# Kernel tuning notes

Measured on AMD Instinct MI355X. Metric: run time of the kernel, lower is better.

The kernel has to match this reference:

```python
import jax, jax.numpy as jnp
import numpy as np

S, L = 4096, 16            # words per sentence, max chars per word
DW, DC, DH = 256, 128, 512  # word emb, char emb, hidden dims
V, A, T = 50000, 128, 64    # vocab, alphabet, tagset sizes


def _lstm_cell(x, h, c, Wih, Whh, bih, bhh):
    # PyTorch LSTM gate math, gate order i, f, g, o
    gates = x @ Wih.T + h @ Whh.T + bih + bhh
    i, f, g, o = jnp.split(gates, 4, axis=-1)
    i, f, o = jax.nn.sigmoid(i), jax.nn.sigmoid(f), jax.nn.sigmoid(o)
    c = f * c + i * jnp.tanh(g)
    h = o * jnp.tanh(c)
    return h, c


def setup_inputs() -> dict:
    key = jax.random.key(0)
    ks = jax.random.split(key, 16)
    s = 0.1
    word_idxs = jax.random.randint(ks[0], (S,), 0, V)
    char_idxs = jax.random.randint(ks[1], (S, L), 0, A)
    char_lens = jnp.maximum(jax.random.randint(ks[2], (S,), 0, L + 1), 1)
    return {
        "word_idxs": word_idxs,
        "char_idxs": char_idxs,
        "char_lens": char_lens,
        "word_emb": jax.random.normal(ks[3], (V, DW)) * s,
        "char_emb": jax.random.normal(ks[4], (A, DC)) * s,
        "Wih_c": jax.random.normal(ks[5], (4 * DC, DC)) * s,
        "Whh_c": jax.random.normal(ks[6], (4 * DC, DC)) * s,
        "bih_c": jnp.zeros((4 * DC,)),
        "bhh_c": jnp.zeros((4 * DC,)),
        "Wih_w": jax.random.normal(ks[7], (4 * DH, DW + DC)) * s,
        "Whh_w": jax.random.normal(ks[8], (4 * DH, DH)) * s,
        "bih_w": jnp.zeros((4 * DH,)),
        "bhh_w": jnp.zeros((4 * DH,)),
        "W_tag": jax.random.normal(ks[9], (T, DH)) * s,
        "b_tag": jnp.zeros((T,)),
    }


def reference(word_idxs, char_idxs, char_lens,
              word_emb, char_emb,
              Wih_c, Whh_c, bih_c, bhh_c,
              Wih_w, Whh_w, bih_w, bhh_w,
              W_tag, b_tag):
    # ---- char-level LSTM, batched over all S words (replaces per-word loop) ----
    cx = char_emb[char_idxs]                 # [S, L, DC]
    cx_t = jnp.swapaxes(cx, 0, 1)            # [L, S, DC], time-major

    def char_step(carry, x_t):
        h, c = carry
        h, c = _lstm_cell(x_t, h, c, Wih_c, Whh_c, bih_c, bhh_c)
        return (h, c), h

    h0 = jnp.zeros((S, DC), cx.dtype)
    _, hs = jax.lax.scan(char_step, (h0, h0), cx_t)   # hs: [L, S, DC]
    hs = jnp.swapaxes(hs, 0, 1)                       # [S, L, DC]
    # original takes lstm_car_out[-1] at the word's true length
    char_feat = jnp.take_along_axis(
        hs, (char_lens - 1)[:, None, None], axis=1)[:, 0, :]   # [S, DC]

    # ---- word-level LSTM over the sentence (batch = 1 in original) ----
    we = word_emb[word_idxs]                          # [S, DW]
    wx = jnp.concatenate([we, char_feat], axis=-1)    # [S, DW+DC]

    def word_step(carry, x_t):
        h, c = carry
        h, c = _lstm_cell(x_t, h, c, Wih_w, Whh_w, bih_w, bhh_w)
        return (h, c), h

    wh0 = jnp.zeros((DH,), wx.dtype)
    _, wout = jax.lax.scan(word_step, (wh0, wh0), wx)  # [S, DH]

    tag_space = wout @ W_tag.T + b_tag                 # [S, T]
    # NOTE: original uses F.log_softmax(tag_space, dim=0) -- over the sequence axis
    return jax.nn.log_softmax(tag_space, axis=0)
```

## Files before the change

### kernel.cpp

```cpp
#include <hip/hip_runtime.h>
#include <hip/hip_bf16.h>


typedef short short8 __attribute__((ext_vector_type(8)));
typedef float f32x4 __attribute__((ext_vector_type(4)));

#define NUM_S 4096
#define NUM_L 16

__device__ __forceinline__ unsigned short f2bf(float f) {
  unsigned x = __float_as_uint(f);
  x += 0x7FFFu + ((x >> 16) & 1u);
  return (unsigned short)(x >> 16);
}
__device__ __forceinline__ uint4 packf8(float4 a, float4 b) {
  uint4 r;
  r.x = (unsigned)f2bf(a.x) | ((unsigned)f2bf(a.y) << 16);
  r.y = (unsigned)f2bf(a.z) | ((unsigned)f2bf(a.w) << 16);
  r.z = (unsigned)f2bf(b.x) | ((unsigned)f2bf(b.y) << 16);
  r.w = (unsigned)f2bf(b.z) | ((unsigned)f2bf(b.w) << 16);
  return r;
}
__device__ __forceinline__ short8 pack_bf8(const float* src) {
  const float4 a = *reinterpret_cast<const float4*>(src);
  const float4 b = *reinterpret_cast<const float4*>(src + 4);
  uint4 u = packf8(a, b);
  union { uint4 u; short8 s; } cv; cv.u = u;
  return cv.s;
}
__device__ __forceinline__ float sigm(float x) { return 1.0f / (1.0f + __expf(-x)); }
__device__ __forceinline__ float tanh_f(float x) {
  x = fminf(15.0f, fmaxf(-15.0f, x));
  float e = __expf(2.0f * x);
  return (e - 1.0f) / (e + 1.0f);
}

__global__ __launch_bounds__(256, 1) void char_lstm_kernel(
    const int* __restrict__ char_idxs,
    const int* __restrict__ char_lens,
    const float* __restrict__ char_emb,
    const float* __restrict__ Wih_c,
    const float* __restrict__ Whh_c,
    const float* __restrict__ bih_c,
    const float* __restrict__ bhh_c,
    float* __restrict__ char_feat)
{
  constexpr int XSTR = 264;
  __shared__ __align__(16) unsigned short X[16 * XSTR];

  const int wg = blockIdx.x;
  const int tid = threadIdx.x;
  const int lane = tid & 63;
  const int wv = tid >> 6;
  const int col = lane & 15;
  const int krow = lane >> 4;

  short8 wfrag[8][8];
#pragma unroll
  for (int p = 0; p < 8; ++p) {
    const int nt = (p >> 1) * 8 + 2 * wv + (p & 1);
    const int n = nt * 16 + col;
#pragma unroll
    for (int kt = 0; kt < 8; ++kt) {
      const int k = kt * 32 + krow * 8;
      const float* src = (kt < 4) ? (Wih_c + n * 128 + k)
                                  : (Whh_c + n * 128 + (k - 128));
      wfrag[p][kt] = pack_bf8(src);
    }
  }
  float bsum[8];
#pragma unroll
  for (int p = 0; p < 8; ++p) {
    const int nt = (p >> 1) * 8 + 2 * wv + (p & 1);
    const int n = nt * 16 + col;
    bsum[p] = bih_c[n] + bhh_c[n];
  }
  int clen[4];
#pragma unroll
  for (int r = 0; r < 4; ++r) clen[r] = char_lens[wg * 16 + krow * 4 + r];

  {
    const int m = tid >> 4, c = tid & 15;
    uint4 z; z.x = z.y = z.z = z.w = 0u;
    *reinterpret_cast<uint4*>(&X[m * XSTR + 128 + c * 8]) = z;
  }
  float cstate[8];
#pragma unroll
  for (int i = 0; i < 8; ++i) cstate[i] = 0.0f;

  for (int l = 0; l < NUM_L; ++l) {
    {
      const int m = tid >> 4, c = tid & 15;
      const int ci = char_idxs[(wg * 16 + m) * NUM_L + l];
      const float4 a = *reinterpret_cast<const float4*>(char_emb + ci * 128 + c * 8);
      const float4 b = *reinterpret_cast<const float4*>(char_emb + ci * 128 + c * 8 + 4);
      *reinterpret_cast<uint4*>(&X[m * XSTR + c * 8]) = packf8(a, b);
    }
    __syncthreads();

    short8 afr[8];
#pragma unroll
    for (int kt = 0; kt < 8; ++kt)
      afr[kt] = *reinterpret_cast<const short8*>(&X[col * XSTR + kt * 32 + krow * 8]);

    f32x4 acc[8];
#pragma unroll
    for (int p = 0; p < 8; ++p) { f32x4 v = {bsum[p], bsum[p], bsum[p], bsum[p]}; acc[p] = v; }
#pragma unroll
    for (int kt = 0; kt < 8; ++kt)
#pragma unroll
      for (int p = 0; p < 8; ++p)
        acc[p] = __builtin_amdgcn_mfma_f32_16x16x32_bf16(afr[kt], wfrag[p][kt], acc[p], 0, 0, 0);
    __syncthreads();

#pragma unroll
    for (int sub = 0; sub < 2; ++sub) {
#pragma unroll
      for (int r = 0; r < 4; ++r) {
        const int m = krow * 4 + r;
        const int d = (2 * wv + sub) * 16 + col;
        const float iv = acc[0 + sub][r];
        const float fv = acc[2 + sub][r];
        const float gv = acc[4 + sub][r];
        const float ov = acc[6 + sub][r];
        const float cc = sigm(fv) * cstate[sub * 4 + r] + sigm(iv) * tanh_f(gv);
        const float hh = sigm(ov) * tanh_f(cc);
        cstate[sub * 4 + r] = cc;
        X[m * XSTR + 128 + d] = (unsigned short)f2bf(hh);
        if (clen[r] == l + 1) char_feat[(wg * 16 + m) * 128 + d] = hh;
      }
    }
  }
}

__global__ __launch_bounds__(256) void cvt_bf16_kernel(
    const float* __restrict__ in, unsigned short* __restrict__ out, int n8) {
  const int i = blockIdx.x * 256 + threadIdx.x;
  if (i < n8) {
    const float4 a = reinterpret_cast<const float4*>(in)[2 * i];
    const float4 b = reinterpret_cast<const float4*>(in)[2 * i + 1];
    reinterpret_cast<uint4*>(out)[i] = packf8(a, b);
  }
}

__global__ __launch_bounds__(256, 1) void word_input_kernel(
    const int* __restrict__ word_idxs,
    const float* __restrict__ word_emb,
    const float* __restrict__ char_feat,
    const unsigned short* __restrict__ wih_bf,
    const float* __restrict__ bih_w,
    const float* __restrict__ bhh_w,
    float* __restrict__ xpart)
{
  constexpr int XSTR = 392;
  __shared__ __align__(16) unsigned short X[64 * XSTR];
  const int wg = blockIdx.x, tid = threadIdx.x;
  const int lane = tid & 63, wv = tid >> 6, col = lane & 15, krow = lane >> 4;
  const int t0 = wg * 64;

#pragma unroll
  for (int rr = 0; rr < 4; ++rr) {
    const int m = rr * 16 + (tid >> 4), c = tid & 15;
    const int widx = word_idxs[t0 + m];
    const float* we = word_emb + (size_t)widx * 256;
    const float4 a0 = *reinterpret_cast<const float4*>(we + c * 8);
    const float4 b0 = *reinterpret_cast<const float4*>(we + c * 8 + 4);
    *reinterpret_cast<uint4*>(&X[m * XSTR + c * 8]) = packf8(a0, b0);
    const float4 a1 = *reinterpret_cast<const float4*>(we + 128 + c * 8);
    const float4 b1 = *reinterpret_cast<const float4*>(we + 128 + c * 8 + 4);
    *reinterpret_cast<uint4*>(&X[m * XSTR + 128 + c * 8]) = packf8(a1, b1);
    const float* cf = char_feat + (size_t)(t0 + m) * 128;
    const float4 a2 = *reinterpret_cast<const float4*>(cf + c * 8);
    const float4 b2 = *reinterpret_cast<const float4*>(cf + c * 8 + 4);
    *reinterpret_cast<uint4*>(&X[m * XSTR + 256 + c * 8]) = packf8(a2, b2);
  }
  __syncthreads();

  short8 afr[4][12];
#pragma unroll
  for (int mt = 0; mt < 4; ++mt)
#pragma unroll
    for (int kt = 0; kt < 12; ++kt)
      afr[mt][kt] = *reinterpret_cast<const short8*>(
          &X[(mt * 16 + col) * XSTR + kt * 32 + krow * 8]);

  for (int nn = 0; nn < 32; ++nn) {
    const int nt = wv * 32 + nn;
    const int n = nt * 16 + col;
    const float bs = bih_w[n] + bhh_w[n];
    f32x4 acc[4];
#pragma unroll
    for (int mt = 0; mt < 4; ++mt) { f32x4 v = {bs, bs, bs, bs}; acc[mt] = v; }
#pragma unroll
    for (int kt = 0; kt < 12; ++kt) {
      const short8 bfr = *reinterpret_cast<const short8*>(
          wih_bf + (size_t)n * 384 + kt * 32 + krow * 8);
#pragma unroll
      for (int mt = 0; mt < 4; ++mt)
        acc[mt] = __builtin_amdgcn_mfma_f32_16x16x32_bf16(afr[mt][kt], bfr, acc[mt], 0, 0, 0);
    }
#pragma unroll
    for (int mt = 0; mt < 4; ++mt)
#pragma unroll
      for (int r = 0; r < 4; ++r)
        xpart[(size_t)(t0 + mt * 16 + krow * 4 + r) * 2048 + n] = acc[mt][r];
  }
}

__global__ __launch_bounds__(512, 1) void word_lstm_kernel(
    const float* __restrict__ Whh_w,
    const float* __restrict__ xpart,
    unsigned* __restrict__ hx)
{
  const int tid = threadIdx.x;
  const int wg = blockIdx.x;
  const int dim = tid >> 4;
  const int gate = (tid >> 2) & 3;
  const int seg = tid & 3;
  const int R = gate * 512 + wg * 32 + dim;

  float4 w4[32];
  {
    const float4* wrow = reinterpret_cast<const float4*>(
        Whh_w + (size_t)R * 512 + seg * 128);
#pragma unroll
    for (int i = 0; i < 32; ++i) w4[i] = wrow[(i + seg) & 31];
  }

  __shared__ __align__(16) float h_lds[2][512];
  __shared__ float glds[128];
  h_lds[0][tid] = 0.0f;
  float creg = 0.0f;
  float xp = (seg == 0) ? xpart[R] : 0.0f;
  __syncthreads();

  for (int t = 0; t < NUM_S; ++t) {
    const int cur = t & 1;

    const float4* h4 = reinterpret_cast<const float4*>(&h_lds[cur][0]) + seg * 32;
    float a0 = 0.0f, a1 = 0.0f;
#pragma unroll
    for (int jj = 0; jj < 32; jj += 2) {
      const int j0 = (jj + seg) & 31;
      const int j1 = (jj + 1 + seg) & 31;
      const float4 hA = h4[j0]; const float4 wA = w4[jj];
      const float4 hB = h4[j1]; const float4 wB = w4[jj + 1];
      a0 = fmaf(wA.x, hA.x, a0); a0 = fmaf(wA.y, hA.y, a0);
      a0 = fmaf(wA.z, hA.z, a0); a0 = fmaf(wA.w, hA.w, a0);
      a1 = fmaf(wB.x, hB.x, a1); a1 = fmaf(wB.y, hB.y, a1);
      a1 = fmaf(wB.z, hB.z, a1); a1 = fmaf(wB.w, hB.w, a1);
    }
    float acc = a0 + a1;
    acc += __shfl_xor(acc, 1, 64);
    acc += __shfl_xor(acc, 2, 64);
    if (seg == 0) {
      glds[gate * 32 + dim] = acc + xp;
      if (t + 1 < NUM_S) xp = xpart[(size_t)(t + 1) * 2048 + R];
    }
    __syncthreads();

    if (tid < 64) {
      unsigned hb = 0u;
      if (tid < 32) {
        const float iv = glds[tid];
        const float fv = glds[32 + tid];
        const float gv = glds[64 + tid];
        const float ov = glds[96 + tid];
        const float cc = sigm(fv) * creg + sigm(iv) * tanh_f(gv);
        const float hh = sigm(ov) * tanh_f(cc);
        creg = cc;
        hb = __float_as_uint(hh) + 0x40000000u;
      }
      const unsigned lo = __shfl(hb, (tid & 15) * 2, 64);
      const unsigned hi = __shfl(hb, (tid & 15) * 2 + 1, 64);
      if (tid < 16) {
        const unsigned long long pv =
            (unsigned long long)lo | ((unsigned long long)hi << 32);
        __hip_atomic_store(
            reinterpret_cast<unsigned long long*>(hx + (size_t)t * 512 + wg * 32) + tid,
            pv, __ATOMIC_RELAXED, __HIP_MEMORY_SCOPE_AGENT);
      }
    }

    if (t + 1 < NUM_S && tid >= 192 && tid < 448) {
      const int c = tid - 192;
      const unsigned long long* p =
          reinterpret_cast<const unsigned long long*>(hx + (size_t)t * 512) + c;
      unsigned long long v =
          __hip_atomic_load(p, __ATOMIC_RELAXED, __HIP_MEMORY_SCOPE_AGENT);
      int guard = 0;
      while (((unsigned)v == 0u || (unsigned)(v >> 32) == 0u) &&
             ++guard < (1 << 20)) {
        v = __hip_atomic_load(p, __ATOMIC_RELAXED, __HIP_MEMORY_SCOPE_AGENT);
      }
      h_lds[cur ^ 1][2 * c]     = __uint_as_float((unsigned)v - 0x40000000u);
      h_lds[cur ^ 1][2 * c + 1] = __uint_as_float((unsigned)(v >> 32) - 0x40000000u);
    }
    __syncthreads();
  }
}

__global__ __launch_bounds__(256, 2) void tag_proj_kernel(
    const unsigned* __restrict__ hx,
    const float* __restrict__ W_tag,
    const float* __restrict__ b_tag,
    float* __restrict__ ts)
{
  __shared__ __align__(16) float wl[4 * 512];
  const int wg = blockIdx.x, tid = threadIdx.x;
  const int s0 = wg * 4;
  {
    const uint4* src = reinterpret_cast<const uint4*>(hx + (size_t)s0 * 512);
    float4* dst = reinterpret_cast<float4*>(wl);
#pragma unroll
    for (int q = 0; q < 2; ++q) {
      const uint4 u = src[q * 256 + tid];
      float4 f;
      f.x = __uint_as_float(u.x - 0x40000000u);
      f.y = __uint_as_float(u.y - 0x40000000u);
      f.z = __uint_as_float(u.z - 0x40000000u);
      f.w = __uint_as_float(u.w - 0x40000000u);
      dst[q * 256 + tid] = f;
    }
  }
  __syncthreads();
  const int c = tid & 63, q = tid >> 6;
  const float4* wt = reinterpret_cast<const float4*>(W_tag + (size_t)c * 512);
  const float4* hr = reinterpret_cast<const float4*>(wl + q * 512);
  float acc = b_tag[c];
#pragma unroll 8
  for (int j = 0; j < 128; ++j) {
    const float4 w = wt[j];
    const float4 h = hr[j];
    acc = fmaf(w.x, h.x, acc);
    acc = fmaf(w.y, h.y, acc);
    acc = fmaf(w.z, h.z, acc);
    acc = fmaf(w.w, h.w, acc);
  }
  ts[(size_t)(s0 + q) * 64 + c] = acc;
}

__global__ __launch_bounds__(256, 1) void softmax_col_kernel(
    const float* __restrict__ ts,
    float* __restrict__ out)
{
  __shared__ float red[4];
  __shared__ float red2[4];
  const int c = blockIdx.x, tid = threadIdx.x;
  float m = -3.4e38f;
  for (int s = tid; s < NUM_S; s += 256) m = fmaxf(m, ts[(size_t)s * 64 + c]);
#pragma unroll
  for (int o = 32; o > 0; o >>= 1) m = fmaxf(m, __shfl_xor(m, o, 64));
  if ((tid & 63) == 0) red[tid >> 6] = m;
  __syncthreads();
  m = fmaxf(fmaxf(red[0], red[1]), fmaxf(red[2], red[3]));
  float sum = 0.0f;
  for (int s = tid; s < NUM_S; s += 256) sum += __expf(ts[(size_t)s * 64 + c] - m);
#pragma unroll
  for (int o = 32; o > 0; o >>= 1) sum += __shfl_xor(sum, o, 64);
  if ((tid & 63) == 0) red2[tid >> 6] = sum;
  __syncthreads();
  sum = red2[0] + red2[1] + red2[2] + red2[3];
  const float L = m + __logf(sum);
  for (int s = tid; s < NUM_S; s += 256)
    out[(size_t)s * 64 + c] = ts[(size_t)s * 64 + c] - L;
}

extern "C" void kernel_launch(void* const* d_in, const int* in_sizes, int n_in,
                              void* d_out, int out_size, void* d_ws, size_t ws_size,
                              hipStream_t stream) {
  (void)in_sizes; (void)n_in; (void)out_size; (void)ws_size;
  const int* word_idxs = (const int*)d_in[0];
  const int* char_idxs = (const int*)d_in[1];
  const int* char_lens = (const int*)d_in[2];
  const float* word_emb = (const float*)d_in[3];
  const float* char_emb = (const float*)d_in[4];
  const float* Wih_c = (const float*)d_in[5];
  const float* Whh_c = (const float*)d_in[6];
  const float* bih_c = (const float*)d_in[7];
  const float* bhh_c = (const float*)d_in[8];
  const float* Wih_w = (const float*)d_in[9];
  const float* Whh_w = (const float*)d_in[10];
  const float* bih_w = (const float*)d_in[11];
  const float* bhh_w = (const float*)d_in[12];
  const float* W_tag = (const float*)d_in[13];
  const float* b_tag = (const float*)d_in[14];

  char* ws = (char*)d_ws;
  float*    xpart  = (float*)(ws);
  unsigned* hx     = (unsigned*)(ws + (size_t)32 * 1024 * 1024);
  float*    cfeat  = (float*)(ws + (size_t)40 * 1024 * 1024);
  float*    ts     = (float*)(ws + (size_t)42 * 1024 * 1024);
  unsigned short* wih_bf = (unsigned short*)(ws + (size_t)43 * 1024 * 1024);

  hipMemsetAsync(hx, 0, (size_t)NUM_S * 512 * sizeof(unsigned), stream);
  cvt_bf16_kernel<<<384, 256, 0, stream>>>(Wih_w, wih_bf, (2048 * 384) / 8);
  char_lstm_kernel<<<256, 256, 0, stream>>>(char_idxs, char_lens, char_emb,
                                            Wih_c, Whh_c, bih_c, bhh_c, cfeat);
  word_input_kernel<<<64, 256, 0, stream>>>(word_idxs, word_emb, cfeat,
                                            wih_bf, bih_w, bhh_w, xpart);
  word_lstm_kernel<<<16, 512, 0, stream>>>(Whh_w, xpart, hx);
  tag_proj_kernel<<<1024, 256, 0, stream>>>(hx, W_tag, b_tag, ts);
  softmax_col_kernel<<<64, 256, 0, stream>>>(ts, (float*)d_out);
}
```

Baseline: 9.166 ms.

## Replace global h broadcast buffer with per-block double-buffered mailboxes

The word LSTM's cross-block hidden-state exchange changes. Each block now pushes its 32 h values into a small per-destination mailbox, double-buffered by step parity, instead of all blocks polling a big per-timestep hx array. Receivers spin on their own mailbox slots, clear them after reading, and write their own slice straight into LDS, while plain h goes to a separate wout buffer for the tag projection. This aims to cut polling latency and cache traffic on the serial critical path, at the cost of 15x more fan-out stores, a threadfence every step, and slot reuse that relies on the clear and parity protocol being correct.

```diff
diff --git a/kernel.cpp b/kernel.cpp
--- a/kernel.cpp
+++ b/kernel.cpp
@@ -210,7 +210,8 @@
 __global__ __launch_bounds__(512, 1) void word_lstm_kernel(
     const float* __restrict__ Whh_w,
     const float* __restrict__ xpart,
-    unsigned* __restrict__ hx)
+    float* __restrict__ wout,
+    unsigned* __restrict__ mbox)
 {
   const int tid = threadIdx.x;
   const int wg = blockIdx.x;
@@ -235,7 +236,7 @@
   __syncthreads();
 
   for (int t = 0; t < NUM_S; ++t) {
-    const int cur = t & 1;
+    const int cur = t & 1, nxt = cur ^ 1, par = t & 1;
 
     const float4* h4 = reinterpret_cast<const float4*>(&h_lds[cur][0]) + seg * 32;
     float a0 = 0.0f, a1 = 0.0f;
@@ -259,49 +260,50 @@
     }
     __syncthreads();
 
-    if (tid < 64) {
-      unsigned hb = 0u;
-      if (tid < 32) {
-        const float iv = glds[tid];
-        const float fv = glds[32 + tid];
-        const float gv = glds[64 + tid];
-        const float ov = glds[96 + tid];
-        const float cc = sigm(fv) * creg + sigm(iv) * tanh_f(gv);
-        const float hh = sigm(ov) * tanh_f(cc);
-        creg = cc;
-        hb = __float_as_uint(hh) + 0x40000000u;
+    if (tid < 32) {
+      const float iv = glds[tid];
+      const float fv = glds[32 + tid];
+      const float gv = glds[64 + tid];
+      const float ov = glds[96 + tid];
+      const float cc = sigm(fv) * creg + sigm(iv) * tanh_f(gv);
+      const float hh = sigm(ov) * tanh_f(cc);
+      creg = cc;
+      wout[(size_t)t * 512 + wg * 32 + tid] = hh;
+      h_lds[nxt][wg * 32 + tid] = hh;
+      if (t + 1 < NUM_S) {
+        const unsigned fb = __float_as_uint(hh) + 0x40000000u;
+        __threadfence();
+#pragma unroll
+        for (int c = 0; c < 16; ++c) {
+          if (c != wg)
+            __hip_atomic_store(mbox + ((size_t)c * 2 + par) * 512 + wg * 32 + tid,
+                               fb, __ATOMIC_RELAXED, __HIP_MEMORY_SCOPE_AGENT);
+        }
       }
-      const unsigned lo = __shfl(hb, (tid & 15) * 2, 64);
-      const unsigned hi = __shfl(hb, (tid & 15) * 2 + 1, 64);
-      if (tid < 16) {
-        const unsigned long long pv =
-            (unsigned long long)lo | ((unsigned long long)hi << 32);
-        __hip_atomic_store(
-            reinterpret_cast<unsigned long long*>(hx + (size_t)t * 512 + wg * 32) + tid,
-            pv, __ATOMIC_RELAXED, __HIP_MEMORY_SCOPE_AGENT);
+    }
+
+    if (t + 1 < NUM_S && tid >= 256) {
+      const int k = tid - 256;
+      if ((k >> 4) != wg) {
+        unsigned long long* p = reinterpret_cast<unsigned long long*>(
+            mbox + ((size_t)wg * 2 + par) * 512) + k;
+        unsigned long long v =
+            __hip_atomic_load(p, __ATOMIC_ACQUIRE, __HIP_MEMORY_SCOPE_AGENT);
+        int guard = 0;
+        while (((unsigned)v == 0u || (unsigned)(v >> 32) == 0u) &&
+               ++guard < (1 << 14))
+          v = __hip_atomic_load(p, __ATOMIC_ACQUIRE, __HIP_MEMORY_SCOPE_AGENT);
+        __hip_atomic_store(p, 0ULL, __ATOMIC_RELAXED, __HIP_MEMORY_SCOPE_AGENT);
+        h_lds[nxt][2 * k]     = __uint_as_float((unsigned)v - 0x40000000u);
+        h_lds[nxt][2 * k + 1] = __uint_as_float((unsigned)(v >> 32) - 0x40000000u);
       }
     }
-
-    if (t + 1 < NUM_S && tid >= 192 && tid < 448) {
-      const int c = tid - 192;
-      const unsigned long long* p =
-          reinterpret_cast<const unsigned long long*>(hx + (size_t)t * 512) + c;
-      unsigned long long v =
-          __hip_atomic_load(p, __ATOMIC_RELAXED, __HIP_MEMORY_SCOPE_AGENT);
-      int guard = 0;
-      while (((unsigned)v == 0u || (unsigned)(v >> 32) == 0u) &&
-             ++guard < (1 << 20)) {
-        v = __hip_atomic_load(p, __ATOMIC_RELAXED, __HIP_MEMORY_SCOPE_AGENT);
-      }
-      h_lds[cur ^ 1][2 * c]     = __uint_as_float((unsigned)v - 0x40000000u);
-      h_lds[cur ^ 1][2 * c + 1] = __uint_as_float((unsigned)(v >> 32) - 0x40000000u);
-    }
     __syncthreads();
   }
 }
 
 __global__ __launch_bounds__(256, 2) void tag_proj_kernel(
-    const unsigned* __restrict__ hx,
+    const float* __restrict__ wout,
     const float* __restrict__ W_tag,
     const float* __restrict__ b_tag,
     float* __restrict__ ts)
@@ -310,18 +312,10 @@
   const int wg = blockIdx.x, tid = threadIdx.x;
   const int s0 = wg * 4;
   {
-    const uint4* src = reinterpret_cast<const uint4*>(hx + (size_t)s0 * 512);
+    const float4* src = reinterpret_cast<const float4*>(wout + (size_t)s0 * 512);
     float4* dst = reinterpret_cast<float4*>(wl);
-#pragma unroll
-    for (int q = 0; q < 2; ++q) {
-      const uint4 u = src[q * 256 + tid];
-      float4 f;
-      f.x = __uint_as_float(u.x - 0x40000000u);
-      f.y = __uint_as_float(u.y - 0x40000000u);
-      f.z = __uint_as_float(u.z - 0x40000000u);
-      f.w = __uint_as_float(u.w - 0x40000000u);
-      dst[q * 256 + tid] = f;
-    }
+    dst[tid] = src[tid];
+    dst[256 + tid] = src[256 + tid];
   }
   __syncthreads();
   const int c = tid & 63, q = tid >> 6;
@@ -388,18 +382,19 @@
 
   char* ws = (char*)d_ws;
   float*    xpart  = (float*)(ws);
-  unsigned* hx     = (unsigned*)(ws + (size_t)32 * 1024 * 1024);
+  float*    wout   = (float*)(ws + (size_t)32 * 1024 * 1024);
   float*    cfeat  = (float*)(ws + (size_t)40 * 1024 * 1024);
   float*    ts     = (float*)(ws + (size_t)42 * 1024 * 1024);
   unsigned short* wih_bf = (unsigned short*)(ws + (size_t)43 * 1024 * 1024);
-
-  hipMemsetAsync(hx, 0, (size_t)NUM_S * 512 * sizeof(unsigned), stream);
+  unsigned* mbox   = (unsigned*)(ws + (size_t)44 * 1024 * 1024 + 512 * 1024);
+
+  hipMemsetAsync(mbox, 0, (size_t)16 * 2 * 512 * sizeof(unsigned), stream);
   cvt_bf16_kernel<<<384, 256, 0, stream>>>(Wih_w, wih_bf, (2048 * 384) / 8);
   char_lstm_kernel<<<256, 256, 0, stream>>>(char_idxs, char_lens, char_emb,
                                             Wih_c, Whh_c, bih_c, bhh_c, cfeat);
   word_input_kernel<<<64, 256, 0, stream>>>(word_idxs, word_emb, cfeat,
                                             wih_bf, bih_w, bhh_w, xpart);
-  word_lstm_kernel<<<16, 512, 0, stream>>>(Whh_w, xpart, hx);
-  tag_proj_kernel<<<1024, 256, 0, stream>>>(hx, W_tag, b_tag, ts);
+  word_lstm_kernel<<<16, 512, 0, stream>>>(Whh_w, xpart, wout, mbox);
+  tag_proj_kernel<<<1024, 256, 0, stream>>>(wout, W_tag, b_tag, ts);
   softmax_col_kernel<<<64, 256, 0, stream>>>(ts, (float*)d_out);
 }
```

After: 13.69 ms. 49.4% more time.
